# Kernel tuning notes

Measured on AMD Instinct MI355X. Metric: run time of the kernel, lower is better.

## Reference

```python
import jax, jax.numpy as jnp
import numpy as np

VOCAB, E, H, HOPS, HEADS = 32000, 128, 256, 3, 4
N, TM, WLEN, TQ = 32, 50, 20, 20


def _gru(x_tbe, h0, Wih, Whh, bih, bhh):
    # x_tbe: [T, B, E] time-major; h0: [B, H]. PyTorch GRU gate order (r, z, n).
    def step(h, xt):
        gi = xt @ Wih.T + bih
        gh = h @ Whh.T + bhh
        ir, iz, inn = jnp.split(gi, 3, axis=-1)
        hr, hz, hn = jnp.split(gh, 3, axis=-1)
        r = jax.nn.sigmoid(ir + hr)
        z = jax.nn.sigmoid(iz + hz)
        n = jnp.tanh(inn + r * hn)
        return (1.0 - z) * n + z * h, None
    h, _ = jax.lax.scan(step, h0, x_tbe)
    return h


def setup_inputs() -> dict:
    key = jax.random.key(0)
    ks = jax.random.split(key, 24)
    f32 = jnp.float32
    emb = jax.random.uniform(ks[0], (VOCAB, E), f32, -3 ** 0.5, 3 ** 0.5)
    emb = emb.at[0].set(0.0)  # padding_idx=0
    s = 0.05
    inp = {
        'stories': jax.random.randint(ks[1], (N, TM, WLEN), 0, VOCAB),
        'questions': jax.random.randint(ks[2], (N, TQ), 0, VOCAB),
        'emb': emb,
        'q_Wih': jax.random.normal(ks[3], (3 * H, E), f32) * s,
        'q_Whh': jax.random.normal(ks[4], (3 * H, H), f32) * s,
        'q_bih': jnp.zeros((3 * H,), f32),
        'q_bhh': jnp.zeros((3 * H,), f32),
        'i_Wih': jax.random.normal(ks[5], (3 * H, E), f32) * s,
        'i_Whh': jax.random.normal(ks[6], (3 * H, H), f32) * s,
        'i_bih': jnp.zeros((3 * H,), f32),
        'i_bhh': jnp.zeros((3 * H,), f32),
        'Wm': jax.random.normal(ks[7], (HOPS, HEADS, H, H), f32) * s,
        'Wo_w': jax.random.normal(ks[8], (HOPS, H, HEADS * H), f32) * s,
        'Wo_b': jnp.full((HOPS, H), 0.01, f32),
        'ft_W1': jax.random.normal(ks[9], (H, H), f32) * s,
        'ft_b1': jnp.full((H,), 0.01, f32),
        'ft_W2': jax.random.normal(ks[10], (H, H), f32) * s,
        'ft_b2': jnp.full((H,), 0.01, f32),
        'g_W1': jax.random.normal(ks[11], (3 * H, 3 * H), f32) * s,
        'g_b1': jnp.full((3 * H,), 0.01, f32),
        'g_W2': jax.random.normal(ks[12], (3 * H, 3 * H), f32) * s,
        'g_b2': jnp.full((3 * H,), 0.01, f32),
        'V_w': jax.random.normal(ks[13], (VOCAB, 3 * H), f32) * s,
    }
    return inp


def reference(stories, questions, emb, q_Wih, q_Whh, q_bih, q_bhh,
              i_Wih, i_Whh, i_bih, i_bhh, Wm, Wo_w, Wo_b,
              ft_W1, ft_b1, ft_W2, ft_b2, g_W1, g_b1, g_W2, g_b2, V_w):
    n, tm, _ = stories.shape
    h = i_Whh.shape[1]
    hops, heads = Wm.shape[0], Wm.shape[1]

    # ---- input module: per-batch-item GRU; hidden state carries across batch items (as in source loop) ----
    story_embs = emb[stories]  # [N, TM, W, E]
    def bstep(hid, se):  # se: [TM, W, E]
        hid2 = _gru(jnp.swapaxes(se, 0, 1), hid, i_Wih, i_Whh, i_bih, i_bhh)
        return hid2, hid2
    _, memory = jax.lax.scan(bstep, jnp.zeros((tm, h), emb.dtype), story_embs)  # [N, TM, H]

    # ---- question module ----
    q_emb = emb[questions]  # [N, TQ, E]
    q = _gru(jnp.swapaxes(q_emb, 0, 1), jnp.zeros((n, h), emb.dtype), q_Wih, q_Whh, q_bih, q_bhh)  # [N, H]

    def ft(x):
        return jax.nn.relu(jax.nn.relu(x @ ft_W1.T + ft_b1) @ ft_W2.T + ft_b2)

    # ---- multi-hop attention controllers ----
    o_k = ft(q)
    buffers = []
    for hp in range(hops):
        proj = jnp.tanh(jnp.einsum('ntd,hed->nhte', memory, Wm[hp]))      # [N,heads,TM,H]
        scores = jax.nn.softmax(jnp.einsum('nhte,ne->nht', proj, o_k), axis=-1)
        rep = jnp.einsum('nht,ntd->nhd', scores, memory)                   # [N,heads,H]
        buf = rep.reshape(n, heads * h) @ Wo_w[hp].T + Wo_b[hp]            # [N,H]
        buffers.append(buf)
        o_k = ft(buf)
    wb = jnp.stack(buffers, axis=1)  # [N, HOPS, H]

    # ---- RM: all-pairs relation MLP (dropout = identity in eval) ----
    npair = hops * hops
    left = jnp.broadcast_to(wb[:, None, :, :], (n, hops, hops, h)).reshape(n, npair, h)
    right = jnp.broadcast_to(wb[:, :, None, :], (n, hops, hops, h)).reshape(n, npair, h)
    qx = jnp.broadcast_to(q[:, None, :], (n, npair, h))
    comb = jnp.concatenate([left, right, qx], axis=-1)                     # [N, HOPS^2, 3H]
    g = jax.nn.relu(jax.nn.relu(comb @ g_W1.T + g_b1) @ g_W2.T + g_b2)
    reasoning = g.sum(axis=1)                                              # [N, 3H]
    return reasoning @ V_w.T                                               # [N, VOCAB]
```

## Files before the change

kernel.cpp:

```cpp
#include <hip/hip_runtime.h>
#include <cmath>

#define VOCABN 32000
#define EE 128
#define HH 256
#define H3 768
#define HOPSN 3
#define HEADSN 4
#define NB 32
#define TMN 50
#define WLENN 20
#define TQN 20
#define NPOS (NB*TMN*WLENN)
#define NQPOS (NB*TQN)

#define OFF_MEM    0
#define OFF_Q      (OFF_MEM + NB*TMN*HH)
#define OFF_OK     (OFF_Q + NB*HH)
#define OFF_WB     (OFF_OK + NB*HH)
#define OFF_REP    (OFF_WB + NB*HOPSN*HH)
#define OFF_REAS   (OFF_REP + NB*HEADSN*HH)
#define OFF_Y1     (OFF_REAS + NB*H3)
#define OFF_GI     (OFF_Y1 + NB*9*H3)

typedef __fp16 h2 __attribute__((ext_vector_type(2)));

__device__ __forceinline__ float sigm(float x) { return 1.f / (1.f + expf(-x)); }

__device__ __forceinline__ unsigned packh2(float x, float y) {
    h2 h = __builtin_amdgcn_cvt_pkrtz(x, y);
    return __builtin_bit_cast(unsigned, h);
}

__device__ __forceinline__ float fdot2u(unsigned a, unsigned b, float c) {
    return __builtin_amdgcn_fdot2(__builtin_bit_cast(h2, a),
                                  __builtin_bit_cast(h2, b), c, false);
}

#define GIB 64
__global__ __launch_bounds__(768) void k_gi(const int* __restrict__ stories,
                                            const int* __restrict__ questions,
                                            const float* __restrict__ emb,
                                            const float* __restrict__ iWih,
                                            const float* __restrict__ qWih,
                                            const float* __restrict__ ibih, const float* __restrict__ ibhh,
                                            const float* __restrict__ qbih, const float* __restrict__ qbhh,
                                            float* __restrict__ ws)
{
    __shared__ unsigned xs[GIB][EE / 2];
    __fp16* __restrict__ gi = (__fp16*)(ws + OFF_GI);
    const int j = threadIdx.x;
    const bool isq = blockIdx.x >= (NPOS / GIB);
    const int pblk = isq ? (blockIdx.x - NPOS / GIB) : blockIdx.x;
    const int p0 = pblk * GIB;
    const size_t g0 = (isq ? (size_t)NPOS : 0) + (size_t)p0;
    const int* __restrict__ toks = isq ? (questions + p0) : (stories + p0);
    const float* __restrict__ Wih = isq ? qWih : iWih;
    const float* __restrict__ bih = isq ? qbih : ibih;
    const float* __restrict__ bhh = isq ? qbhh : ibhh;
    const float bias = (j < 2 * HH) ? (bih[j] + bhh[j]) : bih[j];
    unsigned wreg[EE / 2];
    const float2* wrow = reinterpret_cast<const float2*>(Wih + (size_t)j * EE);
    #pragma unroll
    for (int c = 0; c < EE / 2; ++c) {
        const float2 w2 = wrow[c];
        wreg[c] = packh2(w2.x, w2.y);
    }
    for (int idx = j; idx < GIB * (EE / 2); idx += H3) {
        const int p = idx >> 6, c = idx & 63;
        const int tok = toks[p];
        const float2 e2 = reinterpret_cast<const float2*>(emb + (size_t)tok * EE)[c];
        xs[p][c] = packh2(e2.x, e2.y);
    }
    __syncthreads();
    for (int p = 0; p < GIB; ++p) {
        const uint4* x4 = reinterpret_cast<const uint4*>(&xs[p][0]);
        float acc = bias;
        #pragma unroll
        for (int c4 = 0; c4 < 16; ++c4) {
            const uint4 xv = x4[c4];
            acc = fdot2u(xv.x, wreg[4 * c4 + 0], acc);
            acc = fdot2u(xv.y, wreg[4 * c4 + 1], acc);
            acc = fdot2u(xv.z, wreg[4 * c4 + 2], acc);
            acc = fdot2u(xv.w, wreg[4 * c4 + 3], acc);
        }
        gi[(g0 + p) * H3 + j] = (__fp16)acc;
    }
}

__global__ __launch_bounds__(512, 2) void k_gru5(
    const float* __restrict__ iWhh, const float* __restrict__ qWhh,
    const float* __restrict__ ibhh, const float* __restrict__ qbhh,
    float* __restrict__ ws)
{
    __shared__ unsigned hp32[HH / 2];
    __shared__ float red[HH * 5];
    const int tid = threadIdx.x;
    const int j = tid & 255, kh = tid >> 8;
    const int blk = blockIdx.x;
    const bool isq = blk >= TMN;
    const float* __restrict__ Whh = isq ? qWhh : iWhh;
    unsigned wg0[64], wg1[64], wg2[64];
    {
        const float2* r0 = reinterpret_cast<const float2*>(Whh + (size_t)j * HH + kh * 128);
        const float2* r1 = reinterpret_cast<const float2*>(Whh + (size_t)(HH + j) * HH + kh * 128);
        const float2* r2 = reinterpret_cast<const float2*>(Whh + (size_t)(2 * HH + j) * HH + kh * 128);
        #pragma unroll
        for (int c = 0; c < 64; ++c) { const float2 a = r0[c]; wg0[c] = packh2(a.x, a.y); }
        #pragma unroll
        for (int c = 0; c < 64; ++c) { const float2 a = r1[c]; wg1[c] = packh2(a.x, a.y); }
        #pragma unroll
        for (int c = 0; c < 64; ++c) { const float2 a = r2[c]; wg2[c] = packh2(a.x, a.y); }
    }
    float bnH = 0.f, hstate = 0.f;
    if (kh == 0) bnH = (isq ? qbhh : ibhh)[2 * HH + j];
    if (tid < HH / 2) hp32[tid] = 0u;
    const __fp16* __restrict__ gib = (const __fp16*)(ws + OFF_GI)
                                     + (isq ? (size_t)NPOS * H3 : 0);
    float* __restrict__ memv = ws + OFF_MEM;
    float* __restrict__ qv   = ws + OFF_Q;
    __syncthreads();

    const int nOuter = isq ? 1 : NB;
    const int c = isq ? (blk - TMN) : blk;
    for (int n = 0; n < nOuter; ++n) {
        for (int t = 0; t < WLENN; ++t) {
            const int pos = isq ? (c * TQN + t) : ((n * TMN + c) * WLENN + t);
            float gir = 0.f, giz = 0.f, gin = 0.f;
            if (kh == 0) {
                const size_t gb = (size_t)pos * H3;
                gir = (float)gib[gb + j];
                giz = (float)gib[gb + HH + j];
                gin = (float)gib[gb + 2 * HH + j];
            }
            float a0 = 0.f, a1 = 0.f, a2 = 0.f;
            const uint4* hp4 = reinterpret_cast<const uint4*>(hp32);
            #pragma unroll
            for (int c4 = 0; c4 < 16; ++c4) {
                const uint4 hh = hp4[kh * 16 + c4];
                a0 = fdot2u(hh.x, wg0[4 * c4 + 0], a0);
                a0 = fdot2u(hh.y, wg0[4 * c4 + 1], a0);
                a0 = fdot2u(hh.z, wg0[4 * c4 + 2], a0);
                a0 = fdot2u(hh.w, wg0[4 * c4 + 3], a0);
                a1 = fdot2u(hh.x, wg1[4 * c4 + 0], a1);
                a1 = fdot2u(hh.y, wg1[4 * c4 + 1], a1);
                a1 = fdot2u(hh.z, wg1[4 * c4 + 2], a1);
                a1 = fdot2u(hh.w, wg1[4 * c4 + 3], a1);
                a2 = fdot2u(hh.x, wg2[4 * c4 + 0], a2);
                a2 = fdot2u(hh.y, wg2[4 * c4 + 1], a2);
                a2 = fdot2u(hh.z, wg2[4 * c4 + 2], a2);
                a2 = fdot2u(hh.w, wg2[4 * c4 + 3], a2);
            }
            if (kh == 1) { red[j * 5 + 0] = a0; red[j * 5 + 1] = a1; red[j * 5 + 2] = a2; }
            __syncthreads();
            if (kh == 0) {
                const float* rr = red + j * 5;
                const float r  = sigm(a0 + rr[0] + gir);
                const float z  = sigm(a1 + rr[1] + giz);
                const float nn = tanhf(gin + r * (a2 + rr[2] + bnH));
                hstate = (1.f - z) * nn + z * hstate;
                reinterpret_cast<__fp16*>(hp32)[j] = (__fp16)hstate;
                if (t == WLENN - 1) {
                    if (isq) qv[c * HH + j] = hstate;
                    else     memv[(size_t)(n * TMN + c) * HH + j] = hstate;
                }
            }
            __syncthreads();
        }
    }
}

__global__ __launch_bounds__(256) void k_ft(const float* __restrict__ src, float* __restrict__ dst,
                                            const float* __restrict__ W1, const float* __restrict__ b1,
                                            const float* __restrict__ W2, const float* __restrict__ b2)
{
    __shared__ float xr[HH];
    __shared__ float y1[HH];
    const int n = blockIdx.x, j = threadIdx.x;
    xr[j] = src[n * HH + j];
    __syncthreads();
    float acc = b1[j];
    const float4* w1 = reinterpret_cast<const float4*>(W1 + j * HH);
    #pragma unroll 4
    for (int k4 = 0; k4 < HH / 4; ++k4) {
        const float4 w = w1[k4];
        const float4 x = *reinterpret_cast<const float4*>(&xr[k4 * 4]);
        acc = fmaf(x.x, w.x, fmaf(x.y, w.y, fmaf(x.z, w.z, fmaf(x.w, w.w, acc))));
    }
    y1[j] = fmaxf(acc, 0.f);
    __syncthreads();
    acc = b2[j];
    const float4* w2 = reinterpret_cast<const float4*>(W2 + j * HH);
    #pragma unroll 4
    for (int k4 = 0; k4 < HH / 4; ++k4) {
        const float4 w = w2[k4];
        const float4 x = *reinterpret_cast<const float4*>(&y1[k4 * 4]);
        acc = fmaf(x.x, w.x, fmaf(x.y, w.y, fmaf(x.z, w.z, fmaf(x.w, w.w, acc))));
    }
    dst[n * HH + j] = fmaxf(acc, 0.f);
}

__global__ __launch_bounds__(256) void k_attn(const float* __restrict__ Wm, float* __restrict__ ws, int hp)
{
    __shared__ float mem_s[TMN][HH];
    __shared__ float ok_s[HH];
    __shared__ float wred[4][TMN];
    __shared__ float sc[TMN];
    const int n = blockIdx.x / HEADSN, hh = blockIdx.x % HEADSN;
    const int e = threadIdx.x;
    const float* __restrict__ memory = ws + OFF_MEM + n * TMN * HH;
    for (int idx = e; idx < TMN * HH; idx += HH)
        (&mem_s[0][0])[idx] = memory[idx];
    ok_s[e] = (ws + OFF_OK)[n * HH + e];
    __syncthreads();

    float p[TMN];
    #pragma unroll
    for (int t = 0; t < TMN; ++t) p[t] = 0.f;
    const float4* wrow = reinterpret_cast<const float4*>(Wm + ((size_t)(hp * HEADSN + hh) * HH + e) * HH);
    for (int d4 = 0; d4 < HH / 4; ++d4) {
        const float4 w = wrow[d4];
        #pragma unroll
        for (int t = 0; t < TMN; ++t) {
            const float4 m = *reinterpret_cast<const float4*>(&mem_s[t][d4 * 4]);
            p[t] = fmaf(m.x, w.x, fmaf(m.y, w.y, fmaf(m.z, w.z, fmaf(m.w, w.w, p[t]))));
        }
    }
    const float okv = ok_s[e];
    const int lane = e & 63, wv = e >> 6;
    #pragma unroll
    for (int t = 0; t < TMN; ++t) {
        float v = tanhf(p[t]) * okv;
        #pragma unroll
        for (int off = 32; off > 0; off >>= 1) v += __shfl_xor(v, off);
        if (lane == 0) wred[wv][t] = v;
    }
    __syncthreads();
    if (e < TMN) sc[e] = wred[0][e] + wred[1][e] + wred[2][e] + wred[3][e];
    __syncthreads();
    if (e == 0) {
        float mx = sc[0];
        for (int t = 1; t < TMN; ++t) mx = fmaxf(mx, sc[t]);
        float sum = 0.f;
        for (int t = 0; t < TMN; ++t) { const float ex = expf(sc[t] - mx); sc[t] = ex; sum += ex; }
        const float inv = 1.f / sum;
        for (int t = 0; t < TMN; ++t) sc[t] *= inv;
    }
    __syncthreads();
    float r = 0.f;
    #pragma unroll
    for (int t = 0; t < TMN; ++t) r = fmaf(sc[t], mem_s[t][e], r);
    (ws + OFF_REP)[(n * HEADSN + hh) * HH + e] = r;
}

__global__ __launch_bounds__(256) void k_buf(const float* __restrict__ Wo_w, const float* __restrict__ Wo_b,
                                             const float* __restrict__ W1, const float* __restrict__ b1,
                                             const float* __restrict__ W2, const float* __restrict__ b2,
                                             float* __restrict__ ws, int hp)
{
    __shared__ float repf[HEADSN * HH];
    __shared__ float bufs[HH];
    __shared__ float y1[HH];
    const int n = blockIdx.x, j = threadIdx.x;
    const float* __restrict__ rep = ws + OFF_REP + n * HEADSN * HH;
    for (int idx = j; idx < HEADSN * HH; idx += HH) repf[idx] = rep[idx];
    __syncthreads();
    float acc = Wo_b[hp * HH + j];
    const float4* wrow = reinterpret_cast<const float4*>(Wo_w + ((size_t)hp * HH + j) * (HEADSN * HH));
    #pragma unroll 4
    for (int c4 = 0; c4 < HEADSN * HH / 4; ++c4) {
        const float4 w = wrow[c4];
        const float4 x = *reinterpret_cast<const float4*>(&repf[c4 * 4]);
        acc = fmaf(x.x, w.x, fmaf(x.y, w.y, fmaf(x.z, w.z, fmaf(x.w, w.w, acc))));
    }
    (ws + OFF_WB)[(n * HOPSN + hp) * HH + j] = acc;
    bufs[j] = acc;
    __syncthreads();
    float a1 = b1[j];
    const float4* w1 = reinterpret_cast<const float4*>(W1 + j * HH);
    #pragma unroll 4
    for (int k4 = 0; k4 < HH / 4; ++k4) {
        const float4 w = w1[k4];
        const float4 x = *reinterpret_cast<const float4*>(&bufs[k4 * 4]);
        a1 = fmaf(x.x, w.x, fmaf(x.y, w.y, fmaf(x.z, w.z, fmaf(x.w, w.w, a1))));
    }
    y1[j] = fmaxf(a1, 0.f);
    __syncthreads();
    float a2 = b2[j];
    const float4* w2 = reinterpret_cast<const float4*>(W2 + j * HH);
    #pragma unroll 4
    for (int k4 = 0; k4 < HH / 4; ++k4) {
        const float4 w = w2[k4];
        const float4 x = *reinterpret_cast<const float4*>(&y1[k4 * 4]);
        a2 = fmaf(x.x, w.x, fmaf(x.y, w.y, fmaf(x.z, w.z, fmaf(x.w, w.w, a2))));
    }
    (ws + OFF_OK)[n * HH + j] = fmaxf(a2, 0.f);
}

__global__ __launch_bounds__(256) void k_rm1(const float* __restrict__ gW1, const float* __restrict__ gb1,
                                             float* __restrict__ ws)
{
    __shared__ float comb[9 * H3];
    const int n = blockIdx.x / 3, ot = blockIdx.x % 3;
    const int o = ot * 256 + threadIdx.x;
    const float* __restrict__ wb = ws + OFF_WB + n * HOPSN * HH;
    const float* __restrict__ qv = ws + OFF_Q + n * HH;
    for (int idx = threadIdx.x; idx < 9 * H3; idx += 256) {
        const int p = idx / H3, cc = idx - p * H3;
        const int ii = p / 3, jj = p % 3;
        float v;
        if (cc < HH)           v = wb[jj * HH + cc];
        else if (cc < 2 * HH)  v = wb[ii * HH + (cc - HH)];
        else                   v = qv[cc - 2 * HH];
        comb[idx] = v;
    }
    __syncthreads();
    float acc[9];
    const float b = gb1[o];
    #pragma unroll
    for (int p = 0; p < 9; ++p) acc[p] = b;
    const float4* w1 = reinterpret_cast<const float4*>(gW1 + (size_t)o * H3);
    for (int c4 = 0; c4 < H3 / 4; ++c4) {
        const float4 w = w1[c4];
        #pragma unroll
        for (int p = 0; p < 9; ++p) {
            const float4 x = *reinterpret_cast<const float4*>(&comb[p * H3 + c4 * 4]);
            acc[p] = fmaf(x.x, w.x, fmaf(x.y, w.y, fmaf(x.z, w.z, fmaf(x.w, w.w, acc[p]))));
        }
    }
    float* __restrict__ y1 = ws + OFF_Y1 + (size_t)n * 9 * H3;
    #pragma unroll
    for (int p = 0; p < 9; ++p) y1[p * H3 + o] = fmaxf(acc[p], 0.f);
}

__global__ __launch_bounds__(256) void k_rm2(const float* __restrict__ gW2, const float* __restrict__ gb2,
                                             float* __restrict__ ws)
{
    __shared__ float y1s[9 * H3];
    const int n = blockIdx.x / 3, ot = blockIdx.x % 3;
    const int o = ot * 256 + threadIdx.x;
    const float* __restrict__ y1 = ws + OFF_Y1 + (size_t)n * 9 * H3;
    for (int idx = threadIdx.x; idx < 9 * H3; idx += 256) y1s[idx] = y1[idx];
    __syncthreads();
    float acc[9];
    const float b = gb2[o];
    #pragma unroll
    for (int p = 0; p < 9; ++p) acc[p] = b;
    const float4* w2 = reinterpret_cast<const float4*>(gW2 + (size_t)o * H3);
    for (int c4 = 0; c4 < H3 / 4; ++c4) {
        const float4 w = w2[c4];
        #pragma unroll
        for (int p = 0; p < 9; ++p) {
            const float4 x = *reinterpret_cast<const float4*>(&y1s[p * H3 + c4 * 4]);
            acc[p] = fmaf(x.x, w.x, fmaf(x.y, w.y, fmaf(x.z, w.z, fmaf(x.w, w.w, acc[p]))));
        }
    }
    float s = 0.f;
    #pragma unroll
    for (int p = 0; p < 9; ++p) s += fmaxf(acc[p], 0.f);
    (ws + OFF_REAS)[n * H3 + o] = s;
}

#define RST 36
__global__ __launch_bounds__(256) void k_out(const float* __restrict__ V_w, const float* __restrict__ ws,
                                             float* __restrict__ out)
{
    __shared__ float rsT[H3 * RST];
    const int tid = threadIdx.x;
    const int v = blockIdx.x * 128 + (tid & 127);
    const int nh = tid >> 7;
    for (int idx = tid; idx < NB * H3; idx += 256) {
        const int n = idx / H3, d = idx - n * H3;
        rsT[d * RST + n] = (ws + OFF_REAS)[idx];
    }
    __syncthreads();
    float acc[16];
    #pragma unroll
    for (int i = 0; i < 16; ++i) acc[i] = 0.f;
    const float4* vw = reinterpret_cast<const float4*>(V_w + (size_t)v * H3);
    for (int d4 = 0; d4 < H3 / 4; ++d4) {
        const float4 w = vw[d4];
        #pragma unroll
        for (int dd = 0; dd < 4; ++dd) {
            const float wd = (dd == 0) ? w.x : (dd == 1) ? w.y : (dd == 2) ? w.z : w.w;
            const float* rr = &rsT[(d4 * 4 + dd) * RST + nh * 16];
            #pragma unroll
            for (int q = 0; q < 4; ++q) {
                const float4 r4 = *reinterpret_cast<const float4*>(rr + 4 * q);
                acc[4 * q + 0] = fmaf(wd, r4.x, acc[4 * q + 0]);
                acc[4 * q + 1] = fmaf(wd, r4.y, acc[4 * q + 1]);
                acc[4 * q + 2] = fmaf(wd, r4.z, acc[4 * q + 2]);
                acc[4 * q + 3] = fmaf(wd, r4.w, acc[4 * q + 3]);
            }
        }
    }
    #pragma unroll
    for (int i = 0; i < 16; ++i)
        out[(size_t)(nh * 16 + i) * VOCABN + v] = acc[i];
}

extern "C" void kernel_launch(void* const* d_in, const int* in_sizes, int n_in,
                              void* d_out, int out_size, void* d_ws, size_t ws_size,
                              hipStream_t stream)
{
    const int*   stories   = (const int*)d_in[0];
    const int*   questions = (const int*)d_in[1];
    const float* emb   = (const float*)d_in[2];
    const float* qWih  = (const float*)d_in[3];
    const float* qWhh  = (const float*)d_in[4];
    const float* qbih  = (const float*)d_in[5];
    const float* qbhh  = (const float*)d_in[6];
    const float* iWih  = (const float*)d_in[7];
    const float* iWhh  = (const float*)d_in[8];
    const float* ibih  = (const float*)d_in[9];
    const float* ibhh  = (const float*)d_in[10];
    const float* Wm    = (const float*)d_in[11];
    const float* Wo_w  = (const float*)d_in[12];
    const float* Wo_b  = (const float*)d_in[13];
    const float* ftW1  = (const float*)d_in[14];
    const float* ftb1  = (const float*)d_in[15];
    const float* ftW2  = (const float*)d_in[16];
    const float* ftb2  = (const float*)d_in[17];
    const float* gW1   = (const float*)d_in[18];
    const float* gb1   = (const float*)d_in[19];
    const float* gW2   = (const float*)d_in[20];
    const float* gb2   = (const float*)d_in[21];
    const float* V_w   = (const float*)d_in[22];
    float* ws  = (float*)d_ws;
    float* out = (float*)d_out;

    hipLaunchKernelGGL(k_gi, dim3((NPOS + NQPOS) / GIB), dim3(H3), 0, stream,
                       stories, questions, emb, iWih, qWih, ibih, ibhh, qbih, qbhh, ws);
    hipLaunchKernelGGL(k_gru5, dim3(TMN + NB), dim3(512), 0, stream,
                       iWhh, qWhh, ibhh, qbhh, ws);
    hipLaunchKernelGGL(k_ft, dim3(NB), dim3(HH), 0, stream, ws + OFF_Q, ws + OFF_OK, ftW1, ftb1, ftW2, ftb2);
    for (int hp = 0; hp < HOPSN; ++hp) {
        hipLaunchKernelGGL(k_attn, dim3(NB * HEADSN), dim3(HH), 0, stream, Wm, ws, hp);
        hipLaunchKernelGGL(k_buf, dim3(NB), dim3(HH), 0, stream, Wo_w, Wo_b, ftW1, ftb1, ftW2, ftb2, ws, hp);
    }
    hipLaunchKernelGGL(k_rm1, dim3(NB * 3), dim3(256), 0, stream, gW1, gb1, ws);
    hipLaunchKernelGGL(k_rm2, dim3(NB * 3), dim3(256), 0, stream, gW2, gb2, ws);
    hipLaunchKernelGGL(k_out, dim3(VOCABN / 128), dim3(256), 0, stream, V_w, ws, out);
}
```

Measured before the change: 1.481 ms.

## Hoist memory projections for all hops into one batched kernel before hop loop

```diff
diff --git a/kernel.cpp b/kernel.cpp
--- a/kernel.cpp
+++ b/kernel.cpp
@@ -21,7 +21,8 @@
 #define OFF_REP    (OFF_WB + NB*HOPSN*HH)
 #define OFF_REAS   (OFF_REP + NB*HEADSN*HH)
 #define OFF_Y1     (OFF_REAS + NB*H3)
-#define OFF_GI     (OFF_Y1 + NB*9*H3)
+#define OFF_PROJ   (OFF_Y1 + NB*9*H3)
+#define OFF_GI     (OFF_PROJ + NB*12*TMN*HH)
 
 typedef __fp16 h2 __attribute__((ext_vector_type(2)));
 
@@ -88,7 +89,8 @@
     }
 }
 
-__global__ __launch_bounds__(512, 2) void k_gru5(
+__global__ __attribute__((amdgpu_flat_work_group_size(512, 512), amdgpu_waves_per_eu(2, 2)))
+void k_gru6(
     const float* __restrict__ iWhh, const float* __restrict__ qWhh,
     const float* __restrict__ ibhh, const float* __restrict__ qbhh,
     float* __restrict__ ws)
@@ -200,37 +202,45 @@
     dst[n * HH + j] = fmaxf(acc, 0.f);
 }
 
-__global__ __launch_bounds__(256) void k_attn(const float* __restrict__ Wm, float* __restrict__ ws, int hp)
+__global__ __launch_bounds__(256) void k_proj(const float* __restrict__ Wm, float* __restrict__ ws)
 {
     __shared__ float mem_s[TMN][HH];
-    __shared__ float ok_s[HH];
+    const int n = blockIdx.x / 12, he = blockIdx.x % 12;
+    const int e = threadIdx.x;
+    const float* __restrict__ memory = ws + OFF_MEM + n * TMN * HH;
+    for (int idx = e; idx < TMN * HH; idx += HH)
+        (&mem_s[0][0])[idx] = memory[idx];
+    __syncthreads();
+    float p[TMN];
+    #pragma unroll
+    for (int t = 0; t < TMN; ++t) p[t] = 0.f;
+    const float4* wrow = reinterpret_cast<const float4*>(Wm + ((size_t)he * HH + e) * HH);
+    for (int d4 = 0; d4 < HH / 4; ++d4) {
+        const float4 w = wrow[d4];
+        #pragma unroll
+        for (int t = 0; t < TMN; ++t) {
+            const float4 m = *reinterpret_cast<const float4*>(&mem_s[t][d4 * 4]);
+            p[t] = fmaf(m.x, w.x, fmaf(m.y, w.y, fmaf(m.z, w.z, fmaf(m.w, w.w, p[t]))));
+        }
+    }
+    float* __restrict__ proj = ws + OFF_PROJ + ((size_t)(n * 12 + he) * TMN) * HH;
+    #pragma unroll
+    for (int t = 0; t < TMN; ++t) proj[t * HH + e] = tanhf(p[t]);
+}
+
+__global__ __launch_bounds__(256) void k_attn2(float* __restrict__ ws, int hp)
+{
     __shared__ float wred[4][TMN];
     __shared__ float sc[TMN];
     const int n = blockIdx.x / HEADSN, hh = blockIdx.x % HEADSN;
     const int e = threadIdx.x;
+    const float* __restrict__ proj = ws + OFF_PROJ + ((size_t)(n * 12 + hp * HEADSN + hh) * TMN) * HH;
     const float* __restrict__ memory = ws + OFF_MEM + n * TMN * HH;
-    for (int idx = e; idx < TMN * HH; idx += HH)
-        (&mem_s[0][0])[idx] = memory[idx];
-    ok_s[e] = (ws + OFF_OK)[n * HH + e];
-    __syncthreads();
-
-    float p[TMN];
-    #pragma unroll
-    for (int t = 0; t < TMN; ++t) p[t] = 0.f;
-    const float4* wrow = reinterpret_cast<const float4*>(Wm + ((size_t)(hp * HEADSN + hh) * HH + e) * HH);
-    for (int d4 = 0; d4 < HH / 4; ++d4) {
-        const float4 w = wrow[d4];
-        #pragma unroll
-        for (int t = 0; t < TMN; ++t) {
-            const float4 m = *reinterpret_cast<const float4*>(&mem_s[t][d4 * 4]);
-            p[t] = fmaf(m.x, w.x, fmaf(m.y, w.y, fmaf(m.z, w.z, fmaf(m.w, w.w, p[t]))));
-        }
-    }
-    const float okv = ok_s[e];
+    const float okv = (ws + OFF_OK)[n * HH + e];
     const int lane = e & 63, wv = e >> 6;
-    #pragma unroll
+    #pragma unroll 10
     for (int t = 0; t < TMN; ++t) {
-        float v = tanhf(p[t]) * okv;
+        float v = proj[t * HH + e] * okv;
         #pragma unroll
         for (int off = 32; off > 0; off >>= 1) v += __shfl_xor(v, off);
         if (lane == 0) wred[wv][t] = v;
@@ -248,8 +258,8 @@
     }
     __syncthreads();
     float r = 0.f;
-    #pragma unroll
-    for (int t = 0; t < TMN; ++t) r = fmaf(sc[t], mem_s[t][e], r);
+    #pragma unroll 10
+    for (int t = 0; t < TMN; ++t) r = fmaf(sc[t], memory[t * HH + e], r);
     (ws + OFF_REP)[(n * HEADSN + hh) * HH + e] = r;
 }
 
@@ -431,12 +441,13 @@
 
     hipLaunchKernelGGL(k_gi, dim3((NPOS + NQPOS) / GIB), dim3(H3), 0, stream,
                        stories, questions, emb, iWih, qWih, ibih, ibhh, qbih, qbhh, ws);
-    hipLaunchKernelGGL(k_gru5, dim3(TMN + NB), dim3(512), 0, stream,
+    hipLaunchKernelGGL(k_gru6, dim3(TMN + NB), dim3(512), 0, stream,
                        iWhh, qWhh, ibhh, qbhh, ws);
     hipLaunchKernelGGL(k_ft, dim3(NB), dim3(HH), 0, stream, ws + OFF_Q, ws + OFF_OK, ftW1, ftb1, ftW2, ftb2);
+    hipLaunchKernelGGL(k_proj, dim3(NB * 12), dim3(256), 0, stream, Wm, ws);
     for (int hp = 0; hp < HOPSN; ++hp) {
-        hipLaunchKernelGGL(k_attn, dim3(NB * HEADSN), dim3(HH), 0, stream, Wm, ws, hp);
-        hipLaunchKernelGGL(k_buf, dim3(NB), dim3(HH), 0, stream, Wo_w, Wo_b, ftW1, ftb1, ftW2, ftb2, ws, hp);
+        hipLaunchKernelGGL(k_attn2, dim3(NB * HEADSN), dim3(256), 0, stream, ws, hp);
+        hipLaunchKernelGGL(k_buf, dim3(NB), dim3(256), 0, stream, Wo_w, Wo_b, ftW1, ftb1, ftW2, ftb2, ws, hp);
     }
     hipLaunchKernelGGL(k_rm1, dim3(NB * 3), dim3(256), 0, stream, gW1, gb1, ws);
     hipLaunchKernelGGL(k_rm2, dim3(NB * 3), dim3(256), 0, stream, gW2, gb2, ws);
```

Result: faster. 1.345 ms (-9.2%).
